# Kernel tuning notes

Measured on AMD Instinct MI355X. Metric: run time of the kernel, lower is better.

Reference implementation:

```python
import jax, jax.numpy as jnp
import numpy as np

B, C, H = 16, 256, 128   # batch, channels (in==out, depthwise), spatial
K, S, P = 3, 2, 1        # kernel, stride, padding (the shape-consistent _Transition config)
LEAVES = 4               # levels=2 -> levels**2


def dwconv(x, w, b, stride, pad):
    # depthwise conv: w is [C,1,K,K] (torch OIHW with groups=C)
    out = jax.lax.conv_general_dilated(
        x, w, (stride, stride), [(pad, pad), (pad, pad)],
        dimension_numbers=('NCHW', 'OIHW', 'NCHW'),
        feature_group_count=x.shape[1])
    return out + b[None, :, None, None]


def maxpool(x, k, s, p):
    # matches nn.MaxPool2d (padding acts as -inf for max)
    return jax.lax.reduce_window(
        x, -jnp.inf, jax.lax.max,
        (1, 1, k, k), (1, 1, s, s),
        [(0, 0), (0, 0), (p, p), (p, p)])


def setup_inputs() -> dict:
    key = jax.random.key(0)
    k0, k1, k2, k3 = jax.random.split(key, 4)
    std = (2.0 / (K * K * C)) ** 0.5  # matches the module's normal_(0, sqrt(2/n)) init
    x = jax.random.normal(k0, (B, C, H, H), jnp.float32)
    maxgate = jax.random.normal(k1, (C, 1, K, K), jnp.float32) * std
    pconvs = jax.random.normal(k2, (C, 1, K, K, LEAVES), jnp.float32) * std  # dw=True
    pgates = jax.random.normal(k3, (C, 1, K, K, 3), jnp.float32) * std       # b=False: (leaves+levels)//2 = 3
    mb = jnp.zeros((C,), jnp.float32)
    pbs = jnp.zeros((C, LEAVES), jnp.float32)
    gbs = jnp.zeros((C, 3), jnp.float32)
    return dict(x=x, maxgate=maxgate, mb=mb, pconvs=pconvs, pbs=pbs,
                pgates=pgates, gbs=gbs)


def reference(x, maxgate, mb, pconvs, pbs, pgates, gbs):
    # max branch: maxpool * depthwise gate conv
    out = maxpool(x, K, S, P) * dwconv(x, maxgate, mb, S, P)

    # leaf stage: 2 sigmoid-gated pool pairs (b=False -> gate2 = 1 - gate1)
    # NOTE: code indexes pgates.select(4, c*2) with gbs.select(1, c)
    leaves = []
    for c in range(LEAVES // 2):
        g1 = jax.nn.sigmoid(dwconv(x, pgates[..., 2 * c], gbs[:, c], S, P))
        p1 = dwconv(x, pconvs[..., 2 * c], pbs[:, 2 * c], S, P)
        p2 = dwconv(x, pconvs[..., 2 * c + 1], pbs[:, 2 * c + 1], S, P)
        leaves.append(g1 * p1)
        leaves.append((1.0 - g1) * p2)

    n0 = leaves[0] + leaves[1]
    n1 = leaves[2] + leaves[3]

    # node stage (kernel_size==3 -> no F.pad); b=False reuses pgates[..., leaves//2 + n] = pgates[...,2]
    g = jax.nn.sigmoid(dwconv(n0, pgates[..., LEAVES // 2], gbs[:, 2], 1, P))
    out = out + n0 * g + n1 * (1.0 - g)
    return out
```

## Files before the change

### kernel.cpp

```cpp
#include <hip/hip_runtime.h>
#include <math.h>

#define TB   256
#define HH   128
#define OHW  64
#define TR   8
#define XR   21
#define N0C  68

typedef float f32x2 __attribute__((ext_vector_type(2)));

__device__ __forceinline__ float sigmoidf(float z) {
    return 1.0f / (1.0f + __expf(-z));
}

__device__ __forceinline__ void gl2lds16(const float* g, float* l) {
    __builtin_amdgcn_global_load_lds(
        (const __attribute__((address_space(1))) void*)g,
        (__attribute__((address_space(3))) void*)l, 16, 0, 0);
}
__device__ __forceinline__ void gl2lds4(const float* g, float* l) {
    __builtin_amdgcn_global_load_lds(
        (const __attribute__((address_space(1))) void*)g,
        (__attribute__((address_space(3))) void*)l, 4, 0, 0);
}

__global__ __launch_bounds__(TB, 8) void fused_densenet_kernel(
    const float* __restrict__ x,
    const float* __restrict__ maxgate,
    const float* __restrict__ mb,
    const float* __restrict__ pconvs,
    const float* __restrict__ pbs,
    const float* __restrict__ pgates,
    const float* __restrict__ gbs,
    float* __restrict__ out)
{
    __shared__ float xs[XR][HH];
    __shared__ float n0s[TR + 2][N0C];

    const int t     = threadIdx.x;
    const int lane  = t & 63;
    const int wv    = t >> 6;
    const int bid   = blockIdx.x;
    const int tile  = bid & 7;
    const int plane = bid >> 3;
    const int c     = plane & 255;
    const int r0    = tile * TR;

    float ws[7][9];
#pragma unroll
    for (int i = 0; i < 9; ++i) {
        ws[0][i] = maxgate[c * 9  + i];
        ws[1][i] = pconvs [c * 36 + i * 4 + 0];
        ws[2][i] = pconvs [c * 36 + i * 4 + 1];
        ws[3][i] = pconvs [c * 36 + i * 4 + 2];
        ws[4][i] = pconvs [c * 36 + i * 4 + 3];
        ws[5][i] = pgates [c * 27 + i * 3 + 0];
        ws[6][i] = pgates [c * 27 + i * 3 + 2];
    }
    const float bmax = mb[c];
    const float bp0 = pbs[c * 4 + 0], bp1 = pbs[c * 4 + 1];
    const float bp2 = pbs[c * 4 + 2], bp3 = pbs[c * 4 + 3];
    const float bg0 = gbs[c * 3 + 0];
    const float bg1 = gbs[c * 3 + 1];
    const float bg2 = gbs[c * 3 + 2];

    const float* xplane = x + (size_t)plane * (HH * HH);

    {
        const int ir0  = 2 * r0 - 3;
        const int lo   = ir0 < 0 ? 0 : ir0;
        const int hie  = ir0 + XR - 1;
        const int hi   = hie > HH - 1 ? HH - 1 : hie;
        const int ztop = lo - ir0;
        const int zbot = hie - hi;
        for (int i = t; i < ztop * HH; i += TB) (&xs[0][0])[i] = 0.f;
        for (int i = t; i < zbot * HH; i += TB) (&xs[XR - zbot][0])[i] = 0.f;
        const int    nfl  = (hi - lo + 1) * HH;
        const float* gsrc = xplane + lo * HH;
        float*       ldst = &xs[ztop][0];
        const int nchunk = nfl >> 8;
        for (int k = wv; k < nchunk; k += TB / 64)
            gl2lds16(gsrc + (k << 8) + lane * 4, ldst + (k << 8));
        if ((nfl & 255) && wv == 0) {
            const int off = nchunk << 8;
            gl2lds4(gsrc + off + lane,      ldst + off);
            gl2lds4(gsrc + off + 64 + lane, ldst + off + 64);
        }
        if (t < 2 * (TR + 2)) n0s[t >> 1][(t & 1) ? 66 : 1] = 0.f;
    }
    __syncthreads();

    if (t < 132) {
        const int hb  = (t >= 66);
        const int cc2 = hb ? t - 66 : t;
        const int gc  = cc2 - 1;
        const int gr  = hb ? r0 + TR : r0 - 1;
        float n0v = 0.f;
        if ((unsigned)gr < (unsigned)OHW && (unsigned)gc < (unsigned)OHW) {
            const int sb = hb ? 2 * TR + 2 : 0;
            float ag = 0.f, a0 = 0.f, a1 = 0.f;
#pragma unroll
            for (int dr = 0; dr < 3; ++dr) {
                const float* row = &xs[sb + dr][0];
                const float w0 = (gc > 0) ? row[2 * gc - 1] : 0.f;
                const float w1 = row[2 * gc];
                const float w2 = row[2 * gc + 1];
                ag += w0 * ws[5][3*dr] + w1 * ws[5][3*dr+1] + w2 * ws[5][3*dr+2];
                a0 += w0 * ws[1][3*dr] + w1 * ws[1][3*dr+1] + w2 * ws[1][3*dr+2];
                a1 += w0 * ws[2][3*dr] + w1 * ws[2][3*dr+1] + w2 * ws[2][3*dr+2];
            }
            const float sg = sigmoidf(ag + bg0);
            n0v = sg * (a0 + bp0) + (1.f - sg) * (a1 + bp1);
        }
        n0s[hb ? TR + 1 : 0][cc2 + 1] = n0v;
    }

    const int p  = t & 31;
    const int lr = t >> 5;
    const int gr = r0 + lr;
    float o1a, o1b, n1a, n1b;
    {
        float a[7][2];
#pragma unroll
        for (int ci = 0; ci < 7; ++ci) { a[ci][0] = 0.f; a[ci][1] = 0.f; }
        float mp0 = -INFINITY, mp1 = -INFINITY;
#pragma unroll
        for (int dr = 0; dr < 3; ++dr) {
            const float* row = &xs[2 * lr + 2 + dr][0];
            const float  v0 = (p > 0) ? row[4 * p - 1] : 0.f;
            const float4 vv = *reinterpret_cast<const float4*>(&row[4 * p]);
            const bool rowok = (gr > 0) | (dr > 0);
            const float h0 = fmaxf(fmaxf((p > 0) ? v0 : -INFINITY, vv.x), vv.y);
            const float h1 = fmaxf(fmaxf(vv.y, vv.z), vv.w);
            mp0 = fmaxf(mp0, rowok ? h0 : -INFINITY);
            mp1 = fmaxf(mp1, rowok ? h1 : -INFINITY);
#pragma unroll
            for (int ci = 0; ci < 7; ++ci) {
                a[ci][0] += v0   * ws[ci][3*dr] + vv.x * ws[ci][3*dr+1] + vv.y * ws[ci][3*dr+2];
                a[ci][1] += vv.y * ws[ci][3*dr] + vv.z * ws[ci][3*dr+1] + vv.w * ws[ci][3*dr+2];
            }
        }
        const float sg0a = sigmoidf(a[5][0] + bg0);
        const float sg0b = sigmoidf(a[5][1] + bg0);
        const float n0a = sg0a * (a[1][0] + bp0) + (1.f - sg0a) * (a[2][0] + bp1);
        const float n0b = sg0b * (a[1][1] + bp0) + (1.f - sg0b) * (a[2][1] + bp1);
        *reinterpret_cast<f32x2*>(&n0s[lr + 1][2 * p + 2]) = (f32x2){ n0a, n0b };
        const float sg1a = sigmoidf(a[6][0] + bg1);
        const float sg1b = sigmoidf(a[6][1] + bg1);
        n1a = sg1a * (a[3][0] + bp2) + (1.f - sg1a) * (a[4][0] + bp3);
        n1b = sg1b * (a[3][1] + bp2) + (1.f - sg1b) * (a[4][1] + bp3);
        o1a = mp0 * (a[0][0] + bmax);
        o1b = mp1 * (a[0][1] + bmax);
    }
    __syncthreads();

    {
        float ag0 = 0.f, ag1 = 0.f, n0c0 = 0.f, n0c1 = 0.f;
#pragma unroll
        for (int dr = 0; dr < 3; ++dr) {
            const float e0  = n0s[lr + dr][2 * p + 1];
            const f32x2 mid = *reinterpret_cast<const f32x2*>(&n0s[lr + dr][2 * p + 2]);
            const float e3  = n0s[lr + dr][2 * p + 4];
            ag0 += e0    * ws[6][3*dr] + mid.x * ws[6][3*dr+1] + mid.y * ws[6][3*dr+2];
            ag1 += mid.x * ws[6][3*dr] + mid.y * ws[6][3*dr+1] + e3    * ws[6][3*dr+2];
            if (dr == 1) { n0c0 = mid.x; n0c1 = mid.y; }
        }
        const float ga = sigmoidf(ag0 + bg2);
        const float gb = sigmoidf(ag1 + bg2);
        f32x2 rv;
        rv.x = o1a + n0c0 * ga + n1a * (1.f - ga);
        rv.y = o1b + n0c1 * gb + n1b * (1.f - gb);
        __builtin_nontemporal_store(rv,
            reinterpret_cast<f32x2*>(out + (size_t)plane * (OHW * OHW)
                                     + gr * OHW + 2 * p));
    }
}

extern "C" void kernel_launch(void* const* d_in, const int* in_sizes, int n_in,
                              void* d_out, int out_size, void* d_ws, size_t ws_size,
                              hipStream_t stream) {
    const float* x       = (const float*)d_in[0];
    const float* maxgate = (const float*)d_in[1];
    const float* mb      = (const float*)d_in[2];
    const float* pconvs  = (const float*)d_in[3];
    const float* pbs     = (const float*)d_in[4];
    const float* pgates  = (const float*)d_in[5];
    const float* gbs     = (const float*)d_in[6];
    float* out           = (float*)d_out;

    const int blocks = 16 * 256 * 8;
    fused_densenet_kernel<<<blocks, TB, 0, stream>>>(
        x, maxgate, mb, pconvs, pbs, pgates, gbs, out);
}
```

Before: 94.87 us.

## Process two double-buffered row tiles per block with larger tiles and XCD-aware block mapping

Each block now handles 32 output rows as two 16-row sub-tiles with 512 threads. The second sub-tile's input is staged into a second LDS buffer with async global-to-LDS loads while the first is computed. Block IDs are remapped so that consecutive planes are spread across XCD groups. The aim is to hide load latency and cut per-block setup such as weight loads, at the cost of more LDS per block, lower occupancy, and hand-written waitcnt/barrier sequencing whose correctness depends on the exact count of outstanding vm ops.

```diff
diff --git a/kernel.cpp b/kernel.cpp
--- a/kernel.cpp
+++ b/kernel.cpp
@@ -1,12 +1,14 @@
 #include <hip/hip_runtime.h>
 #include <math.h>
 
-#define TB   256
+#define TB   512
 #define HH   128
 #define OHW  64
-#define TR   8
-#define XR   21
+#define TR   16
+#define XR   37
 #define N0C  68
+#define NBLK (16 * 256 * 2)
+#define CPX  (NBLK / 8)
 
 typedef float f32x2 __attribute__((ext_vector_type(2)));
 
@@ -25,7 +27,30 @@
         (__attribute__((address_space(3))) void*)l, 4, 0, 0);
 }
 
-__global__ __launch_bounds__(TB, 8) void fused_densenet_kernel(
+__device__ __forceinline__ void stage_sub(float* buf, const float* xplane,
+                                          int r0s, int t, int wv, int lane) {
+    const int ir0  = 2 * r0s - 3;
+    const int lo   = ir0 < 0 ? 0 : ir0;
+    const int hie  = ir0 + XR - 1;
+    const int hi   = hie > HH - 1 ? HH - 1 : hie;
+    const int ztop = lo - ir0;
+    const int zbot = hie - hi;
+    for (int i = t; i < ztop * HH; i += TB) buf[i] = 0.f;
+    for (int i = t; i < zbot * HH; i += TB) buf[(XR - zbot) * HH + i] = 0.f;
+    const int    nfl  = (hi - lo + 1) * HH;
+    const float* gsrc = xplane + lo * HH;
+    float*       ldst = buf + ztop * HH;
+    const int nchunk = nfl >> 8;
+    for (int k = wv; k < nchunk; k += TB / 64)
+        gl2lds16(gsrc + (k << 8) + lane * 4, ldst + (k << 8));
+    if ((nfl & 255) && wv == 0) {
+        const int off = nchunk << 8;
+        gl2lds4(gsrc + off + lane,      ldst + off);
+        gl2lds4(gsrc + off + 64 + lane, ldst + off + 64);
+    }
+}
+
+__global__ __launch_bounds__(TB, 6) void fused_densenet_kernel(
     const float* __restrict__ x,
     const float* __restrict__ maxgate,
     const float* __restrict__ mb,
@@ -35,17 +60,18 @@
     const float* __restrict__ gbs,
     float* __restrict__ out)
 {
-    __shared__ float xs[XR][HH];
+    __shared__ float xs[2][XR][HH];
     __shared__ float n0s[TR + 2][N0C];
 
     const int t     = threadIdx.x;
     const int lane  = t & 63;
     const int wv    = t >> 6;
     const int bid   = blockIdx.x;
-    const int tile  = bid & 7;
-    const int plane = bid >> 3;
+    const int l     = (bid & 7) * CPX + (bid >> 3);
+    const int pair  = l & 1;
+    const int plane = l >> 1;
     const int c     = plane & 255;
-    const int r0    = tile * TR;
+    const int r0b   = pair * 2 * TR;
 
     float ws[7][9];
 #pragma unroll
@@ -66,114 +92,110 @@
     const float bg2 = gbs[c * 3 + 2];
 
     const float* xplane = x + (size_t)plane * (HH * HH);
-
-    {
-        const int ir0  = 2 * r0 - 3;
-        const int lo   = ir0 < 0 ? 0 : ir0;
-        const int hie  = ir0 + XR - 1;
-        const int hi   = hie > HH - 1 ? HH - 1 : hie;
-        const int ztop = lo - ir0;
-        const int zbot = hie - hi;
-        for (int i = t; i < ztop * HH; i += TB) (&xs[0][0])[i] = 0.f;
-        for (int i = t; i < zbot * HH; i += TB) (&xs[XR - zbot][0])[i] = 0.f;
-        const int    nfl  = (hi - lo + 1) * HH;
-        const float* gsrc = xplane + lo * HH;
-        float*       ldst = &xs[ztop][0];
-        const int nchunk = nfl >> 8;
-        for (int k = wv; k < nchunk; k += TB / 64)
-            gl2lds16(gsrc + (k << 8) + lane * 4, ldst + (k << 8));
-        if ((nfl & 255) && wv == 0) {
-            const int off = nchunk << 8;
-            gl2lds4(gsrc + off + lane,      ldst + off);
-            gl2lds4(gsrc + off + 64 + lane, ldst + off + 64);
-        }
-        if (t < 2 * (TR + 2)) n0s[t >> 1][(t & 1) ? 66 : 1] = 0.f;
-    }
+    float*       oplane = out + (size_t)plane * (OHW * OHW);
+
+    stage_sub(&xs[0][0][0], xplane, r0b, t, wv, lane);
+    if (t < 2 * (TR + 2)) n0s[t >> 1][(t & 1) ? 66 : 1] = 0.f;
     __syncthreads();
 
-    if (t < 132) {
-        const int hb  = (t >= 66);
-        const int cc2 = hb ? t - 66 : t;
-        const int gc  = cc2 - 1;
-        const int gr  = hb ? r0 + TR : r0 - 1;
-        float n0v = 0.f;
-        if ((unsigned)gr < (unsigned)OHW && (unsigned)gc < (unsigned)OHW) {
-            const int sb = hb ? 2 * TR + 2 : 0;
-            float ag = 0.f, a0 = 0.f, a1 = 0.f;
+    const int p   = t & 31;
+    const int row = t >> 5;
+
+#pragma unroll
+    for (int s = 0; s < 2; ++s) {
+        const int r0 = r0b + s * TR;
+        const float* buf = &xs[s][0][0];
+
+        if (s == 0)
+            stage_sub(&xs[1][0][0], xplane, r0b + TR, t, wv, lane);
+
+        if (t < 132) {
+            const int hb  = (t >= 66);
+            const int cc2 = hb ? t - 66 : t;
+            const int gc  = cc2 - 1;
+            const int gr  = hb ? r0 + TR : r0 - 1;
+            float n0v = 0.f;
+            if ((unsigned)gr < (unsigned)OHW && (unsigned)gc < (unsigned)OHW) {
+                const int sb = hb ? 2 * TR + 2 : 0;
+                float ag = 0.f, a0 = 0.f, a1 = 0.f;
+#pragma unroll
+                for (int dr = 0; dr < 3; ++dr) {
+                    const float* rw = buf + (sb + dr) * HH;
+                    const float w0 = (gc > 0) ? rw[2 * gc - 1] : 0.f;
+                    const float w1 = rw[2 * gc];
+                    const float w2 = rw[2 * gc + 1];
+                    ag += w0 * ws[5][3*dr] + w1 * ws[5][3*dr+1] + w2 * ws[5][3*dr+2];
+                    a0 += w0 * ws[1][3*dr] + w1 * ws[1][3*dr+1] + w2 * ws[1][3*dr+2];
+                    a1 += w0 * ws[2][3*dr] + w1 * ws[2][3*dr+1] + w2 * ws[2][3*dr+2];
+                }
+                const float sg = sigmoidf(ag + bg0);
+                n0v = sg * (a0 + bp0) + (1.f - sg) * (a1 + bp1);
+            }
+            n0s[hb ? TR + 1 : 0][cc2 + 1] = n0v;
+        }
+
+        const int gr = r0 + row;
+        float o1a, o1b, n1a, n1b;
+        {
+            float a[7][2];
+#pragma unroll
+            for (int ci = 0; ci < 7; ++ci) { a[ci][0] = 0.f; a[ci][1] = 0.f; }
+            float mp0 = -INFINITY, mp1 = -INFINITY;
 #pragma unroll
             for (int dr = 0; dr < 3; ++dr) {
-                const float* row = &xs[sb + dr][0];
-                const float w0 = (gc > 0) ? row[2 * gc - 1] : 0.f;
-                const float w1 = row[2 * gc];
-                const float w2 = row[2 * gc + 1];
-                ag += w0 * ws[5][3*dr] + w1 * ws[5][3*dr+1] + w2 * ws[5][3*dr+2];
-                a0 += w0 * ws[1][3*dr] + w1 * ws[1][3*dr+1] + w2 * ws[1][3*dr+2];
-                a1 += w0 * ws[2][3*dr] + w1 * ws[2][3*dr+1] + w2 * ws[2][3*dr+2];
+                const float* rw = buf + (2 * row + 2 + dr) * HH;
+                const float  v0 = (p > 0) ? rw[4 * p - 1] : 0.f;
+                const float4 vv = *reinterpret_cast<const float4*>(&rw[4 * p]);
+                const bool rowok = (gr > 0) | (dr > 0);
+                const float h0 = fmaxf(fmaxf((p > 0) ? v0 : -INFINITY, vv.x), vv.y);
+                const float h1 = fmaxf(fmaxf(vv.y, vv.z), vv.w);
+                mp0 = fmaxf(mp0, rowok ? h0 : -INFINITY);
+                mp1 = fmaxf(mp1, rowok ? h1 : -INFINITY);
+#pragma unroll
+                for (int ci = 0; ci < 7; ++ci) {
+                    a[ci][0] += v0   * ws[ci][3*dr] + vv.x * ws[ci][3*dr+1] + vv.y * ws[ci][3*dr+2];
+                    a[ci][1] += vv.y * ws[ci][3*dr] + vv.z * ws[ci][3*dr+1] + vv.w * ws[ci][3*dr+2];
+                }
             }
-            const float sg = sigmoidf(ag + bg0);
-            n0v = sg * (a0 + bp0) + (1.f - sg) * (a1 + bp1);
-        }
-        n0s[hb ? TR + 1 : 0][cc2 + 1] = n0v;
-    }
-
-    const int p  = t & 31;
-    const int lr = t >> 5;
-    const int gr = r0 + lr;
-    float o1a, o1b, n1a, n1b;
-    {
-        float a[7][2];
-#pragma unroll
-        for (int ci = 0; ci < 7; ++ci) { a[ci][0] = 0.f; a[ci][1] = 0.f; }
-        float mp0 = -INFINITY, mp1 = -INFINITY;
-#pragma unroll
-        for (int dr = 0; dr < 3; ++dr) {
-            const float* row = &xs[2 * lr + 2 + dr][0];
-            const float  v0 = (p > 0) ? row[4 * p - 1] : 0.f;
-            const float4 vv = *reinterpret_cast<const float4*>(&row[4 * p]);
-            const bool rowok = (gr > 0) | (dr > 0);
-            const float h0 = fmaxf(fmaxf((p > 0) ? v0 : -INFINITY, vv.x), vv.y);
-            const float h1 = fmaxf(fmaxf(vv.y, vv.z), vv.w);
-            mp0 = fmaxf(mp0, rowok ? h0 : -INFINITY);
-            mp1 = fmaxf(mp1, rowok ? h1 : -INFINITY);
-#pragma unroll
-            for (int ci = 0; ci < 7; ++ci) {
-                a[ci][0] += v0   * ws[ci][3*dr] + vv.x * ws[ci][3*dr+1] + vv.y * ws[ci][3*dr+2];
-                a[ci][1] += vv.y * ws[ci][3*dr] + vv.z * ws[ci][3*dr+1] + vv.w * ws[ci][3*dr+2];
+            const float sg0a = sigmoidf(a[5][0] + bg0);
+            const float sg0b = sigmoidf(a[5][1] + bg0);
+            const float n0a = sg0a * (a[1][0] + bp0) + (1.f - sg0a) * (a[2][0] + bp1);
+            const float n0b = sg0b * (a[1][1] + bp0) + (1.f - sg0b) * (a[2][1] + bp1);
+            *reinterpret_cast<f32x2*>(&n0s[row + 1][2 * p + 2]) = (f32x2){ n0a, n0b };
+            const float sg1a = sigmoidf(a[6][0] + bg1);
+            const float sg1b = sigmoidf(a[6][1] + bg1);
+            n1a = sg1a * (a[3][0] + bp2) + (1.f - sg1a) * (a[4][0] + bp3);
+            n1b = sg1b * (a[3][1] + bp2) + (1.f - sg1b) * (a[4][1] + bp3);
+            o1a = mp0 * (a[0][0] + bmax);
+            o1b = mp1 * (a[0][1] + bmax);
+        }
+
+        asm volatile("s_waitcnt lgkmcnt(0)\n\ts_barrier" ::: "memory");
+
+        {
+            float ag0 = 0.f, ag1 = 0.f, n0c0 = 0.f, n0c1 = 0.f;
+#pragma unroll
+            for (int dr = 0; dr < 3; ++dr) {
+                const float e0  = n0s[row + dr][2 * p + 1];
+                const f32x2 mid = *reinterpret_cast<const f32x2*>(&n0s[row + dr][2 * p + 2]);
+                const float e3  = n0s[row + dr][2 * p + 4];
+                ag0 += e0    * ws[6][3*dr] + mid.x * ws[6][3*dr+1] + mid.y * ws[6][3*dr+2];
+                ag1 += mid.x * ws[6][3*dr] + mid.y * ws[6][3*dr+1] + e3    * ws[6][3*dr+2];
+                if (dr == 1) { n0c0 = mid.x; n0c1 = mid.y; }
             }
-        }
-        const float sg0a = sigmoidf(a[5][0] + bg0);
-        const float sg0b = sigmoidf(a[5][1] + bg0);
-        const float n0a = sg0a * (a[1][0] + bp0) + (1.f - sg0a) * (a[2][0] + bp1);
-        const float n0b = sg0b * (a[1][1] + bp0) + (1.f - sg0b) * (a[2][1] + bp1);
-        *reinterpret_cast<f32x2*>(&n0s[lr + 1][2 * p + 2]) = (f32x2){ n0a, n0b };
-        const float sg1a = sigmoidf(a[6][0] + bg1);
-        const float sg1b = sigmoidf(a[6][1] + bg1);
-        n1a = sg1a * (a[3][0] + bp2) + (1.f - sg1a) * (a[4][0] + bp3);
-        n1b = sg1b * (a[3][1] + bp2) + (1.f - sg1b) * (a[4][1] + bp3);
-        o1a = mp0 * (a[0][0] + bmax);
-        o1b = mp1 * (a[0][1] + bmax);
-    }
-    __syncthreads();
-
-    {
-        float ag0 = 0.f, ag1 = 0.f, n0c0 = 0.f, n0c1 = 0.f;
-#pragma unroll
-        for (int dr = 0; dr < 3; ++dr) {
-            const float e0  = n0s[lr + dr][2 * p + 1];
-            const f32x2 mid = *reinterpret_cast<const f32x2*>(&n0s[lr + dr][2 * p + 2]);
-            const float e3  = n0s[lr + dr][2 * p + 4];
-            ag0 += e0    * ws[6][3*dr] + mid.x * ws[6][3*dr+1] + mid.y * ws[6][3*dr+2];
-            ag1 += mid.x * ws[6][3*dr] + mid.y * ws[6][3*dr+1] + e3    * ws[6][3*dr+2];
-            if (dr == 1) { n0c0 = mid.x; n0c1 = mid.y; }
-        }
-        const float ga = sigmoidf(ag0 + bg2);
-        const float gb = sigmoidf(ag1 + bg2);
-        f32x2 rv;
-        rv.x = o1a + n0c0 * ga + n1a * (1.f - ga);
-        rv.y = o1b + n0c1 * gb + n1b * (1.f - gb);
-        __builtin_nontemporal_store(rv,
-            reinterpret_cast<f32x2*>(out + (size_t)plane * (OHW * OHW)
-                                     + gr * OHW + 2 * p));
+            const float ga = sigmoidf(ag0 + bg2);
+            const float gb = sigmoidf(ag1 + bg2);
+            f32x2 rv;
+            rv.x = o1a + n0c0 * ga + n1a * (1.f - ga);
+            rv.y = o1b + n0c1 * gb + n1b * (1.f - gb);
+            __builtin_nontemporal_store(rv,
+                reinterpret_cast<f32x2*>(oplane + gr * OHW + 2 * p));
+        }
+
+        if (s == 0) {
+            asm volatile("s_waitcnt vmcnt(1)" ::: "memory");
+            __builtin_amdgcn_s_barrier();
+        }
     }
 }
 
@@ -189,7 +211,6 @@
     const float* gbs     = (const float*)d_in[6];
     float* out           = (float*)d_out;
 
-    const int blocks = 16 * 256 * 8;
-    fused_densenet_kernel<<<blocks, TB, 0, stream>>>(
+    fused_densenet_kernel<<<NBLK, TB, 0, stream>>>(
         x, maxgate, mb, pconvs, pbs, pgates, gbs, out);
 }
```

Result: faster. 90.10 us (-5.0%).
